# Optimization experiments

Measured on AMD Instinct MI355X. Metric: run time of the kernel, lower is better.

The kernel has to match this reference:

```python
import jax, jax.numpy as jnp
import numpy as np

B, N, D = 2, 2048, 2048
H, HKV, HD = 16, 4, 128  # n_heads, n_kv_heads, head_dim
G = H // HKV             # GQA group size


def setup_inputs() -> dict:
    key = jax.random.key(0)
    ks = jax.random.split(key, 5)
    x = jax.random.normal(ks[0], (B, N, D), jnp.float32)
    # rotary angles: standard 10000-base frequencies, half head_dim
    inv_freq = 1.0 / (10000.0 ** (jnp.arange(HD // 2, dtype=jnp.float32) / (HD // 2)))
    ang = jnp.arange(N, dtype=jnp.float32)[:, None] * inv_freq[None, :]  # [N, HD/2]
    cos = jnp.cos(ang)[None, :, None, :]  # [1, N, 1, HD/2]
    sin = jnp.sin(ang)[None, :, None, :]
    attn_mask = jnp.ones((B, N), jnp.float32)
    s = 0.02
    Wq = jax.random.normal(ks[1], (D, H * HD), jnp.float32) * s
    Wkv = jax.random.normal(ks[2], (D, 2 * HKV * HD), jnp.float32) * s
    Wo = jax.random.normal(ks[3], (H * HD, D), jnp.float32) * s
    bo = jnp.zeros((D,), jnp.float32)
    return {"x": x, "cos": cos, "sin": sin, "attn_mask": attn_mask,
            "Wq": Wq, "Wkv": Wkv, "Wo": Wo, "bo": bo}


def _rope(t, cos, sin):
    # t: [b, n, h, d]; rotate-half style split at d//2
    d2 = t.shape[-1] // 2
    t1, t2 = t[..., :d2], t[..., d2:]
    return jnp.concatenate([t1 * cos + t2 * sin, t2 * cos - t1 * sin], axis=-1)


def reference(x, cos, sin, attn_mask, Wq, Wkv, Wo, bo):
    b, n, _ = x.shape
    q = (x @ Wq).reshape(b, n, H, HD)
    kv = x @ Wkv
    k, v = jnp.split(kv, 2, axis=-1)
    k = k.reshape(b, n, HKV, HD)
    v = v.reshape(b, n, HKV, HD)
    q = _rope(q, cos, sin)
    k = _rope(k, cos, sin)
    # b n h d -> b h n d; group q heads: head H_idx maps to kv head H_idx % HKV
    # (einops '(r h)' repeat pattern => q reshaped as [b, G, HKV, n, d])
    q = q.transpose(0, 2, 1, 3).reshape(b, G, HKV, n, HD)
    k = k.transpose(0, 2, 1, 3)  # [b, HKV, n, d]
    v = v.transpose(0, 2, 1, 3)
    scale = HD ** -0.5
    attn = jnp.einsum('bghnd,bhmd->bghnm', q, k) * scale
    bias = (1.0 - attn_mask) * -1e9  # [b, n_keys]
    attn = attn + bias[:, None, None, None, :]
    attn = jax.nn.softmax(attn, axis=-1)
    out = jnp.einsum('bghnm,bhmd->bghnd', attn, v)
    # b (g h) n d -> b n (g h d)
    out = out.transpose(0, 3, 1, 2, 4).reshape(b, n, H * HD)
    return out @ Wo + bo
```

## Files before the change

### kernel.cpp

```cpp
#include <hip/hip_runtime.h>
#include <hip/hip_bf16.h>
#include <cstddef>

#define NB    2
#define NSEQ  2048
#define DMODEL 2048
#define NH    16
#define NKV   4
#define HDIM  128

typedef __attribute__((ext_vector_type(8))) short short8;
typedef __attribute__((ext_vector_type(4))) short short4v;
typedef __attribute__((ext_vector_type(4))) float floatx4;
typedef const __attribute__((address_space(1))) void* gptr_t;
typedef __attribute__((address_space(3))) void* lptr_t;

#if __has_builtin(__builtin_amdgcn_exp2f)
#define EXP2F(x) __builtin_amdgcn_exp2f(x)
#else
#define EXP2F(x) __expf((x) * 0.6931471805599453f)
#endif

__device__ inline unsigned short f2bf(float f) {
    unsigned int u = __float_as_uint(f);
    u += 0x7fffu + ((u >> 16) & 1u);
    return (unsigned short)(u >> 16);
}

__device__ inline unsigned int pk2bf_trunc(float a, float b) {
    return __builtin_amdgcn_perm(__float_as_uint(b), __float_as_uint(a), 0x07060302u);
}

__device__ inline floatx4 fzero4() {
    floatx4 v; v[0] = 0.f; v[1] = 0.f; v[2] = 0.f; v[3] = 0.f; return v;
}

__global__ void prep_k(const float* __restrict__ x, const float* __restrict__ Wq,
                       const float* __restrict__ Wkv, const float* __restrict__ Wo,
                       const float* __restrict__ mask,
                       unsigned short* __restrict__ xb,
                       unsigned short* __restrict__ W1T,
                       unsigned short* __restrict__ WoT,
                       float* __restrict__ bias2) {
    __shared__ float tile[32][33];
    const int bid = blockIdx.x, t = threadIdx.x;
    if (bid < 8192) {
        int i = bid * 256 + t;
        float4 v = ((const float4*)x)[i];
        ushort4 o;
        o.x = f2bf(v.x); o.y = f2bf(v.y); o.z = f2bf(v.z); o.w = f2bf(v.w);
        ((ushort4*)xb)[i] = o;
        return;
    }
    if (bid >= 18432) {
        int i = (bid - 18432) * 1024 + t * 4;
        float4 m = *(const float4*)(mask + i);
        const float c = -1.4426950408889634e9f;
        float4 o;
        o.x = (1.f - m.x) * c; o.y = (1.f - m.y) * c;
        o.z = (1.f - m.z) * c; o.w = (1.f - m.w) * c;
        *(float4*)(bias2 + i) = o;
        return;
    }
    const float* W; unsigned short* Wt; int N, local;
    if (bid < 12288)      { W = Wq;  Wt = W1T;                       N = 2048; local = bid - 8192; }
    else if (bid < 14336) { W = Wkv; Wt = W1T + (size_t)2048 * 2048; N = 1024; local = bid - 12288; }
    else                  { W = Wo;  Wt = WoT;                       N = 2048; local = bid - 14336; }
    const int K = 2048;
    int nt = N >> 5;
    int bx = local % nt, by = local / nt;
    int n0 = bx * 32, k0 = by * 32, tx = t & 31, ty = t >> 5;
#pragma unroll
    for (int i = 0; i < 4; i++)
        tile[ty + i * 8][tx] = W[(size_t)(k0 + ty + i * 8) * N + n0 + tx];
    __syncthreads();
#pragma unroll
    for (int i = 0; i < 4; i++)
        Wt[(size_t)(n0 + ty + i * 8) * K + k0 + tx] = f2bf(tile[tx][ty + i * 8]);
}

__global__ __launch_bounds__(256, 3) void gemm_bt(
    const unsigned short* __restrict__ A,
    const unsigned short* __restrict__ Bt,
    float* __restrict__ C,
    const float* __restrict__ bias,
    int M, int N, int K) {
    __shared__ __align__(16) unsigned short As[128 * 64];
    __shared__ __align__(16) unsigned short Bs[128 * 64];
    const int t = threadIdx.x;
    const int chunk = gridDim.x >> 3;
    const int wgid = (blockIdx.x & 7) * chunk + (blockIdx.x >> 3);
    const int nx = N >> 7;
    const int m0 = (wgid / nx) * 128, n0 = (wgid % nx) * 128;
    const int lane = t & 63, wave = t >> 6;
    const int ln = lane & 15, quad = lane >> 4;
    const int wm = (wave >> 1) * 64, wn = (wave & 1) * 64;
    floatx4 acc[4][4];
#pragma unroll
    for (int r = 0; r < 4; r++)
#pragma unroll
        for (int c = 0; c < 4; c++) acc[r][c] = fzero4();

    int xsw[2];
#pragma unroll
    for (int kc = 0; kc < 2; kc++)
        xsw[kc] = (((kc << 2) + quad) ^ (ln & 7)) * 8;

    for (int kt = 0; kt < K; kt += 64) {
#pragma unroll
        for (int i = 0; i < 4; i++) {
            int c = i * 256 + t, r = c >> 3, c8 = c & 7;
            int scol = kt + ((c8 ^ (r & 7)) * 8);
            __builtin_amdgcn_global_load_lds(
                (gptr_t)(A + (size_t)(m0 + r) * K + scol),
                (lptr_t)(As + c * 8), 16, 0, 0);
            __builtin_amdgcn_global_load_lds(
                (gptr_t)(Bt + (size_t)(n0 + r) * K + scol),
                (lptr_t)(Bs + c * 8), 16, 0, 0);
        }
        __syncthreads();
#pragma unroll
        for (int kc = 0; kc < 2; kc++) {
            short8 af[4], bfr[4];
#pragma unroll
            for (int r = 0; r < 4; r++)
                af[r] = *(const short8*)(As + (wm + r * 16 + ln) * 64 + xsw[kc]);
#pragma unroll
            for (int c = 0; c < 4; c++)
                bfr[c] = *(const short8*)(Bs + (wn + c * 16 + ln) * 64 + xsw[kc]);
#pragma unroll
            for (int r = 0; r < 4; r++)
#pragma unroll
                for (int c = 0; c < 4; c++)
                    acc[r][c] = __builtin_amdgcn_mfma_f32_16x16x32_bf16(
                        af[r], bfr[c], acc[r][c], 0, 0, 0);
        }
        __syncthreads();
    }
#pragma unroll
    for (int r = 0; r < 4; r++) {
        int mb = m0 + wm + r * 16 + quad * 4;
#pragma unroll
        for (int c = 0; c < 4; c++) {
            int col = n0 + wn + c * 16 + ln;
            float bv = bias ? bias[col] : 0.f;
#pragma unroll
            for (int g = 0; g < 4; g++)
                C[(size_t)(mb + g) * N + col] = acc[r][c][g] + bv;
        }
    }
}

__global__ __launch_bounds__(256, 3) void gemm_qkv_rope(
    const unsigned short* __restrict__ A,
    const unsigned short* __restrict__ Bt,
    const float* __restrict__ cosb,
    const float* __restrict__ sinb,
    unsigned short* __restrict__ Qb,
    unsigned short* __restrict__ Kb,
    unsigned short* __restrict__ Vt) {
    const int K = DMODEL;
    __shared__ __align__(16) unsigned char smem[128 * 136 * 2];
    unsigned short* As = (unsigned short*)smem;
    unsigned short* Bs = (unsigned short*)(smem + 16384);
    unsigned short* Vx = (unsigned short*)smem;
    const int t = threadIdx.x;
    const int wgid = (blockIdx.x & 7) * 96 + (blockIdx.x >> 3);
    const int m0 = (wgid / 24) * 128, n0 = (wgid % 24) * 128;
    const int lane = t & 63, wave = t >> 6;
    const int ln = lane & 15, quad = lane >> 4;
    const int wm = (wave >> 1) * 64, bq = (wave & 1) * 32;
    floatx4 acc[4][4];
#pragma unroll
    for (int r = 0; r < 4; r++)
#pragma unroll
        for (int c = 0; c < 4; c++) acc[r][c] = fzero4();

    int xsw[2];
#pragma unroll
    for (int kc = 0; kc < 2; kc++)
        xsw[kc] = (((kc << 2) + quad) ^ (ln & 7)) * 8;

    for (int kt = 0; kt < K; kt += 64) {
#pragma unroll
        for (int i = 0; i < 4; i++) {
            int c = i * 256 + t, r = c >> 3, c8 = c & 7;
            int scol = kt + ((c8 ^ (r & 7)) * 8);
            __builtin_amdgcn_global_load_lds(
                (gptr_t)(A + (size_t)(m0 + r) * K + scol),
                (lptr_t)(As + c * 8), 16, 0, 0);
            __builtin_amdgcn_global_load_lds(
                (gptr_t)(Bt + (size_t)(n0 + r) * K + scol),
                (lptr_t)(Bs + c * 8), 16, 0, 0);
        }
        __syncthreads();
#pragma unroll
        for (int kc = 0; kc < 2; kc++) {
            short8 af[4], bfr[4];
#pragma unroll
            for (int r = 0; r < 4; r++)
                af[r] = *(const short8*)(As + (wm + r * 16 + ln) * 64 + xsw[kc]);
#pragma unroll
            for (int c = 0; c < 4; c++)
                bfr[c] = *(const short8*)(
                    Bs + (bq + (c & 1) * 16 + (c >> 1) * 64 + ln) * 64 + xsw[kc]);
#pragma unroll
            for (int r = 0; r < 4; r++)
#pragma unroll
                for (int c = 0; c < 4; c++)
                    acc[r][c] = __builtin_amdgcn_mfma_f32_16x16x32_bf16(
                        af[r], bfr[c], acc[r][c], 0, 0, 0);
        }
        __syncthreads();
    }

    if (n0 < 2048) {
        const float qs = (float)(0.08838834764831845 * 1.4426950408889634);
        int h = n0 >> 7;
#pragma unroll
        for (int r = 0; r < 4; r++)
#pragma unroll
            for (int c = 0; c < 2; c++)
#pragma unroll
                for (int g = 0; g < 4; g++) {
                    int row = m0 + wm + r * 16 + quad * 4 + g;
                    int b = row >> 11, n = row & 2047;
                    int j = bq + c * 16 + ln;
                    float cv = cosb[n * 64 + j], sv = sinb[n * 64 + j];
                    float t1 = acc[r][c][g], t2 = acc[r][c + 2][g];
                    unsigned short* qp = Qb + ((size_t)(b * NH + h) * NSEQ + n) * 128;
                    qp[j]      = f2bf((t1 * cv + t2 * sv) * qs);
                    qp[j + 64] = f2bf((t2 * cv - t1 * sv) * qs);
                }
    } else if (n0 < 2560) {
        int hk = (n0 - 2048) >> 7;
#pragma unroll
        for (int r = 0; r < 4; r++)
#pragma unroll
            for (int c = 0; c < 2; c++)
#pragma unroll
                for (int g = 0; g < 4; g++) {
                    int row = m0 + wm + r * 16 + quad * 4 + g;
                    int b = row >> 11, n = row & 2047;
                    int j = bq + c * 16 + ln;
                    float cv = cosb[n * 64 + j], sv = sinb[n * 64 + j];
                    float t1 = acc[r][c][g], t2 = acc[r][c + 2][g];
                    unsigned short* kp = Kb + ((size_t)(b * NKV + hk) * NSEQ + n) * 128;
                    kp[j]      = f2bf(t1 * cv + t2 * sv);
                    kp[j + 64] = f2bf(t2 * cv - t1 * sv);
                }
    } else {
        int hk = (n0 - 2560) >> 7;
#pragma unroll
        for (int r = 0; r < 4; r++)
#pragma unroll
            for (int c = 0; c < 4; c++) {
                int d = bq + (c & 1) * 16 + (c >> 1) * 64 + ln;
                int s = wm + (r >> 1) * 32 + quad * 8 + (r & 1) * 4;
#pragma unroll
                for (int g = 0; g < 4; g++)
                    Vx[d * 136 + s + g] = f2bf(acc[r][c][g]);
            }
        __syncthreads();
        int b = m0 >> 11, nloc = m0 & 2047;
#pragma unroll
        for (int pass = 0; pass < 2; pass++) {
            int d = pass * 64 + (t >> 2), q4 = t & 3;
            unsigned short* vp =
                Vt + ((size_t)(b * NKV + hk) * 128 + d) * NSEQ + nloc + q4 * 32;
#pragma unroll
            for (int i = 0; i < 4; i++)
                *(short8*)(vp + i * 8) = *(const short8*)(Vx + d * 136 + q4 * 32 + i * 8);
        }
    }
}

__global__ __launch_bounds__(128, 2) void attn_k(
    const unsigned short* __restrict__ Qb,
    const unsigned short* __restrict__ Kb,
    const unsigned short* __restrict__ Vt,
    const float* __restrict__ bias2,
    unsigned short* __restrict__ Ab) {
    __shared__ __align__(16) unsigned short Ks[2 * 32 * 128];
    __shared__ __align__(16) unsigned short Vs[2 * 128 * 32];
    const int t = threadIdx.x, wave = t >> 6, lane = t & 63;
    const int ln = lane & 15, quad = lane >> 4;
    const int id = blockIdx.x;
    const int pair = id & 7, b = pair >> 2, kv = pair & 3;
    const int rest = id >> 3, g4 = rest & 3, h = g4 * 4 + kv, qb = rest >> 2;
    const int q0 = qb * 64;

    const unsigned short* Kbase = Kb + (size_t)(b * NKV + kv) * NSEQ * 128;
    const unsigned short* Vbase = Vt + (size_t)(b * NKV + kv) * 128 * NSEQ;
    const float* bbase = bias2 + b * NSEQ;

    const unsigned short* Qp =
        Qb + ((size_t)(b * NH + h) * NSEQ + q0 + wave * 32 + ln) * 128;
    short8 qf[2][4];
#pragma unroll
    for (int rt = 0; rt < 2; rt++)
#pragma unroll
        for (int kc = 0; kc < 4; kc++)
            qf[rt][kc] = *(const short8*)(Qp + rt * 16 * 128 + kc * 32 + quad * 8);

    const char* kp[4];
#pragma unroll
    for (int kc = 0; kc < 4; kc++)
        kp[kc] = (const char*)Ks + ln * 256 + (((kc * 4 + quad) ^ (ln & 7)) * 16);
    const char* vpp = (const char*)Vs + ln * 64 + ((quad ^ ((ln ^ (ln >> 2)) & 3)) * 16);

    floatx4 Oacc[2][8];
#pragma unroll
    for (int rt = 0; rt < 2; rt++)
#pragma unroll
        for (int d = 0; d < 8; d++) Oacc[rt][d] = fzero4();
    floatx4 Lacc[2];
    Lacc[0] = fzero4(); Lacc[1] = fzero4();

    short8 ones8;
#pragma unroll
    for (int i = 0; i < 8; i++) ones8[i] = (short)0x3F80;

    auto stage = [&](int ktn, int buf) {
#pragma unroll
        for (int i = 0; i < 4; i++) {
            int c = i * 128 + t, r = c >> 4, c8 = c & 15;
            __builtin_amdgcn_global_load_lds(
                (gptr_t)(Kbase + (size_t)(ktn + r) * 128 + ((c8 ^ (r & 7)) * 8)),
                (lptr_t)(Ks + buf * 4096 + c * 8), 16, 0, 0);
        }
#pragma unroll
        for (int i = 0; i < 4; i++) {
            int c = i * 128 + t, dr = c >> 2, c8 = c & 3;
            int f = (dr ^ (dr >> 2)) & 3;
            __builtin_amdgcn_global_load_lds(
                (gptr_t)(Vbase + (size_t)dr * NSEQ + ktn + ((c8 ^ f) * 8)),
                (lptr_t)(Vs + buf * 4096 + c * 8), 16, 0, 0);
        }
    };

    stage(0, 0);
    __syncthreads();

#pragma unroll 1
    for (int it2 = 0; it2 < NSEQ / 64; ++it2) {
#pragma unroll
        for (int half = 0; half < 2; ++half) {
            const int kt = (it2 * 2 + half) * 32;
            const int ktn = (kt + 32) & (NSEQ - 1);
            stage(ktn, half ^ 1);
            const int off = half * 8192;

            floatx4 sacc[2][2];
#pragma unroll
            for (int nj = 0; nj < 2; nj++) {
                floatx4 bv = *(const floatx4*)(bbase + kt + nj * 16 + quad * 4);
                sacc[0][nj] = bv;
                sacc[1][nj] = bv;
            }
            __builtin_amdgcn_s_setprio(1);
#pragma unroll
            for (int kc = 0; kc < 4; kc++) {
                short8 kfv[2];
#pragma unroll
                for (int nj = 0; nj < 2; nj++)
                    kfv[nj] = *(const short8*)(kp[kc] + off + nj * 4096);
#pragma unroll
                for (int rt = 0; rt < 2; rt++)
#pragma unroll
                    for (int nj = 0; nj < 2; nj++)
                        sacc[rt][nj] = __builtin_amdgcn_mfma_f32_16x16x32_bf16(
                            kfv[nj], qf[rt][kc], sacc[rt][nj], 0, 0, 0);
            }
            __builtin_amdgcn_s_setprio(0);

            short8 pf[2];
#pragma unroll
            for (int rt = 0; rt < 2; rt++) {
                union { short8 s; unsigned int w[4]; } pu;
#pragma unroll
                for (int e = 0; e < 2; e++) {
                    float e0 = EXP2F(sacc[rt][e][0]);
                    float e1 = EXP2F(sacc[rt][e][1]);
                    float e2 = EXP2F(sacc[rt][e][2]);
                    float e3 = EXP2F(sacc[rt][e][3]);
                    pu.w[e * 2 + 0] = pk2bf_trunc(e0, e1);
                    pu.w[e * 2 + 1] = pk2bf_trunc(e2, e3);
                }
                pf[rt] = pu.s;
            }

            __builtin_amdgcn_s_setprio(1);
#pragma unroll
            for (int rt = 0; rt < 2; rt++)
                Lacc[rt] = __builtin_amdgcn_mfma_f32_16x16x32_bf16(
                    ones8, pf[rt], Lacc[rt], 0, 0, 0);
#pragma unroll
            for (int dt = 0; dt < 8; dt++) {
                short8 vf = *(const short8*)(vpp + off + dt * 1024);
#pragma unroll
                for (int rt = 0; rt < 2; rt++)
                    Oacc[rt][dt] = __builtin_amdgcn_mfma_f32_16x16x32_bf16(
                        vf, pf[rt], Oacc[rt][dt], 0, 0, 0);
            }
            __builtin_amdgcn_s_setprio(0);
            __syncthreads();
        }
    }

#pragma unroll
    for (int rt = 0; rt < 2; rt++) {
        float inv = 1.f / Lacc[rt][0];
        int row = q0 + wave * 32 + rt * 16 + ln;
        unsigned short* outp = Ab + (size_t)(b * NSEQ + row) * 2048 + h * 128;
#pragma unroll
        for (int dt = 0; dt < 8; dt++) {
            short4v o4;
#pragma unroll
            for (int g = 0; g < 4; g++) o4[g] = (short)f2bf(Oacc[rt][dt][g] * inv);
            *(short4v*)(outp + dt * 16 + quad * 4) = o4;
        }
    }
}

extern "C" void kernel_launch(void* const* d_in, const int* in_sizes, int n_in,
                              void* d_out, int out_size, void* d_ws, size_t ws_size,
                              hipStream_t stream) {
    const float* x    = (const float*)d_in[0];
    const float* cosb = (const float*)d_in[1];
    const float* sinb = (const float*)d_in[2];
    const float* mask = (const float*)d_in[3];
    const float* Wq   = (const float*)d_in[4];
    const float* Wkv  = (const float*)d_in[5];
    const float* Wo   = (const float*)d_in[6];
    const float* bo   = (const float*)d_in[7];
    float* out = (float*)d_out;

    char* ws = (char*)d_ws;
    unsigned short* xb  = (unsigned short*)ws; ws += (size_t)4096 * 2048 * 2;
    unsigned short* W1T = (unsigned short*)ws; ws += (size_t)3072 * 2048 * 2;
    unsigned short* WoT = (unsigned short*)ws; ws += (size_t)2048 * 2048 * 2;
    unsigned short* Qb  = (unsigned short*)ws; ws += (size_t)2 * 16 * 2048 * 128 * 2;
    unsigned short* Kb  = (unsigned short*)ws; ws += (size_t)2 * 4 * 2048 * 128 * 2;
    unsigned short* Vt  = (unsigned short*)ws; ws += (size_t)2 * 4 * 2048 * 128 * 2;
    unsigned short* Ab  = (unsigned short*)ws; ws += (size_t)2 * 2048 * 2048 * 2;
    float* bias2 = (float*)ws;                 ws += (size_t)NB * NSEQ * 4;

    prep_k<<<18436, 256, 0, stream>>>(x, Wq, Wkv, Wo, mask, xb, W1T, WoT, bias2);
    gemm_qkv_rope<<<768, 256, 0, stream>>>(xb, W1T, cosb, sinb, Qb, Kb, Vt);
    attn_k<<<1024, 128, 0, stream>>>(Qb, Kb, Vt, bias2, Ab);
    gemm_bt<<<512, 256, 0, stream>>>(Ab, WoT, out, bo, 4096, 2048, 2048);
}
```

Measured before the change: 300.7 us.

## Use 512x128 tiles with triple-buffered async LDS pipeline in both GEMMs

Both projection GEMMs move to 512-thread workgroups computing 512x128 output tiles with a K-step of 32. Operands are staged through a three-slot LDS ring filled by global_load_lds, using partial vmcnt waits and raw barriers so loads overlap MFMA work, plus s_setprio around the math. This trades occupancy and grid size (192 and 128 blocks, fewer than the CU count) for more operand reuse per block and latency hiding. The V-transpose epilogue is redone in four passes to fit the larger tile.

```diff
diff --git a/kernel.cpp b/kernel.cpp
--- a/kernel.cpp
+++ b/kernel.cpp
@@ -79,79 +79,100 @@
         Wt[(size_t)(n0 + ty + i * 8) * K + k0 + tx] = f2bf(tile[tx][ty + i * 8]);
 }
 
-__global__ __launch_bounds__(256, 3) void gemm_bt(
+
+__global__ __launch_bounds__(512) void gemm_bt(
     const unsigned short* __restrict__ A,
     const unsigned short* __restrict__ Bt,
     float* __restrict__ C,
     const float* __restrict__ bias,
     int M, int N, int K) {
-    __shared__ __align__(16) unsigned short As[128 * 64];
-    __shared__ __align__(16) unsigned short Bs[128 * 64];
+    __shared__ __align__(16) unsigned short As[3 * 512 * 32];
+    __shared__ __align__(16) unsigned short Bs[3 * 128 * 32];
     const int t = threadIdx.x;
     const int chunk = gridDim.x >> 3;
     const int wgid = (blockIdx.x & 7) * chunk + (blockIdx.x >> 3);
     const int nx = N >> 7;
-    const int m0 = (wgid / nx) * 128, n0 = (wgid % nx) * 128;
+    const int m0 = (wgid / nx) * 512, n0 = (wgid % nx) * 128;
     const int lane = t & 63, wave = t >> 6;
     const int ln = lane & 15, quad = lane >> 4;
-    const int wm = (wave >> 1) * 64, wn = (wave & 1) * 64;
-    floatx4 acc[4][4];
-#pragma unroll
-    for (int r = 0; r < 4; r++)
+    const int wm = (wave >> 1) * 128, bq = (wave & 1) * 32;
+    const int xrd = (quad ^ (ln & 3) ^ ((ln >> 2) & 3)) * 8;
+    floatx4 acc[8][4];
+#pragma unroll
+    for (int r = 0; r < 8; r++)
 #pragma unroll
         for (int c = 0; c < 4; c++) acc[r][c] = fzero4();
 
-    int xsw[2];
-#pragma unroll
-    for (int kc = 0; kc < 2; kc++)
-        xsw[kc] = (((kc << 2) + quad) ^ (ln & 7)) * 8;
-
-    for (int kt = 0; kt < K; kt += 64) {
-#pragma unroll
-        for (int i = 0; i < 4; i++) {
-            int c = i * 256 + t, r = c >> 3, c8 = c & 7;
-            int scol = kt + ((c8 ^ (r & 7)) * 8);
-            __builtin_amdgcn_global_load_lds(
-                (gptr_t)(A + (size_t)(m0 + r) * K + scol),
-                (lptr_t)(As + c * 8), 16, 0, 0);
-            __builtin_amdgcn_global_load_lds(
-                (gptr_t)(Bt + (size_t)(n0 + r) * K + scol),
-                (lptr_t)(Bs + c * 8), 16, 0, 0);
-        }
-        __syncthreads();
-#pragma unroll
-        for (int kc = 0; kc < 2; kc++) {
-            short8 af[4], bfr[4];
-#pragma unroll
-            for (int r = 0; r < 4; r++)
-                af[r] = *(const short8*)(As + (wm + r * 16 + ln) * 64 + xsw[kc]);
-#pragma unroll
-            for (int c = 0; c < 4; c++)
-                bfr[c] = *(const short8*)(Bs + (wn + c * 16 + ln) * 64 + xsw[kc]);
-#pragma unroll
-            for (int r = 0; r < 4; r++)
-#pragma unroll
-                for (int c = 0; c < 4; c++)
-                    acc[r][c] = __builtin_amdgcn_mfma_f32_16x16x32_bf16(
-                        af[r], bfr[c], acc[r][c], 0, 0, 0);
-        }
-        __syncthreads();
-    }
-#pragma unroll
-    for (int r = 0; r < 4; r++) {
+    auto stage = [&](int kt, int buf) {
+#pragma unroll
+        for (int j = 0; j < 4; ++j) {
+            int c = j * 512 + t, r = c >> 2, c4 = c & 3;
+            int sx = (c4 ^ (r & 3) ^ ((r >> 2) & 3)) * 8;
+            __builtin_amdgcn_global_load_lds(
+                (gptr_t)(A + (size_t)(m0 + r) * K + kt + sx),
+                (lptr_t)(As + buf * 16384 + c * 8), 16, 0, 0);
+        }
+        {
+            int c = t, r = c >> 2, c4 = c & 3;
+            int sx = (c4 ^ (r & 3) ^ ((r >> 2) & 3)) * 8;
+            __builtin_amdgcn_global_load_lds(
+                (gptr_t)(Bt + (size_t)(n0 + r) * K + kt + sx),
+                (lptr_t)(Bs + buf * 4096 + c * 8), 16, 0, 0);
+        }
+    };
+
+    stage(0, 0);
+    stage(32, 1);
+    asm volatile("s_waitcnt vmcnt(5)" ::: "memory");
+    __builtin_amdgcn_s_barrier();
+
+    int cur = 0, tgt = 2;
+#pragma unroll 1
+    for (int i = 0; i < K / 32; ++i) {
+        const int ktn = ((i + 2) * 32) & (K - 1);
+        stage(ktn, tgt);
+        const unsigned short* Ab_ = As + cur * 16384;
+        const unsigned short* Bb_ = Bs + cur * 4096;
+        short8 bfr[4];
+#pragma unroll
+        for (int c = 0; c < 4; ++c)
+            bfr[c] = *(const short8*)(Ab_ - Ab_ + Bb_ + (bq + (c & 1) * 16 + (c >> 1) * 64 + ln) * 32 + xrd);
+        __builtin_amdgcn_s_setprio(1);
+#pragma unroll
+        for (int ha = 0; ha < 2; ++ha) {
+            short8 af[4];
+#pragma unroll
+            for (int rr = 0; rr < 4; ++rr)
+                af[rr] = *(const short8*)(Ab_ + (wm + (ha * 4 + rr) * 16 + ln) * 32 + xrd);
+#pragma unroll
+            for (int rr = 0; rr < 4; ++rr)
+#pragma unroll
+                for (int c = 0; c < 4; ++c)
+                    acc[ha * 4 + rr][c] = __builtin_amdgcn_mfma_f32_16x16x32_bf16(
+                        af[rr], bfr[c], acc[ha * 4 + rr][c], 0, 0, 0);
+        }
+        __builtin_amdgcn_s_setprio(0);
+        asm volatile("s_waitcnt vmcnt(5)" ::: "memory");
+        __builtin_amdgcn_s_barrier();
+        cur = (cur == 2) ? 0 : cur + 1;
+        tgt = (tgt == 2) ? 0 : tgt + 1;
+    }
+
+#pragma unroll
+    for (int r = 0; r < 8; ++r) {
         int mb = m0 + wm + r * 16 + quad * 4;
 #pragma unroll
-        for (int c = 0; c < 4; c++) {
-            int col = n0 + wn + c * 16 + ln;
+        for (int c = 0; c < 4; ++c) {
+            int col = n0 + bq + (c & 1) * 16 + (c >> 1) * 64 + ln;
             float bv = bias ? bias[col] : 0.f;
 #pragma unroll
-            for (int g = 0; g < 4; g++)
+            for (int g = 0; g < 4; ++g)
                 C[(size_t)(mb + g) * N + col] = acc[r][c][g] + bv;
         }
     }
 }
 
-__global__ __launch_bounds__(256, 3) void gemm_qkv_rope(
+__global__ __launch_bounds__(512) void gemm_qkv_rope(
     const unsigned short* __restrict__ A,
     const unsigned short* __restrict__ Bt,
     const float* __restrict__ cosb,
@@ -160,65 +181,83 @@
     unsigned short* __restrict__ Kb,
     unsigned short* __restrict__ Vt) {
     const int K = DMODEL;
-    __shared__ __align__(16) unsigned char smem[128 * 136 * 2];
+    __shared__ __align__(16) unsigned char smem[122880];
     unsigned short* As = (unsigned short*)smem;
-    unsigned short* Bs = (unsigned short*)(smem + 16384);
+    unsigned short* Bs = (unsigned short*)(smem + 98304);
     unsigned short* Vx = (unsigned short*)smem;
     const int t = threadIdx.x;
-    const int wgid = (blockIdx.x & 7) * 96 + (blockIdx.x >> 3);
-    const int m0 = (wgid / 24) * 128, n0 = (wgid % 24) * 128;
+    const int wgid = (blockIdx.x & 7) * 24 + (blockIdx.x >> 3);
+    const int m0 = (wgid / 24) * 512, n0 = (wgid % 24) * 128;
     const int lane = t & 63, wave = t >> 6;
     const int ln = lane & 15, quad = lane >> 4;
-    const int wm = (wave >> 1) * 64, bq = (wave & 1) * 32;
-    floatx4 acc[4][4];
-#pragma unroll
-    for (int r = 0; r < 4; r++)
+    const int wm = (wave >> 1) * 128, bq = (wave & 1) * 32;
+    const int xrd = (quad ^ (ln & 3) ^ ((ln >> 2) & 3)) * 8;
+    floatx4 acc[8][4];
+#pragma unroll
+    for (int r = 0; r < 8; r++)
 #pragma unroll
         for (int c = 0; c < 4; c++) acc[r][c] = fzero4();
 
-    int xsw[2];
-#pragma unroll
-    for (int kc = 0; kc < 2; kc++)
-        xsw[kc] = (((kc << 2) + quad) ^ (ln & 7)) * 8;
-
-    for (int kt = 0; kt < K; kt += 64) {
-#pragma unroll
-        for (int i = 0; i < 4; i++) {
-            int c = i * 256 + t, r = c >> 3, c8 = c & 7;
-            int scol = kt + ((c8 ^ (r & 7)) * 8);
-            __builtin_amdgcn_global_load_lds(
-                (gptr_t)(A + (size_t)(m0 + r) * K + scol),
-                (lptr_t)(As + c * 8), 16, 0, 0);
-            __builtin_amdgcn_global_load_lds(
-                (gptr_t)(Bt + (size_t)(n0 + r) * K + scol),
-                (lptr_t)(Bs + c * 8), 16, 0, 0);
-        }
-        __syncthreads();
-#pragma unroll
-        for (int kc = 0; kc < 2; kc++) {
-            short8 af[4], bfr[4];
-#pragma unroll
-            for (int r = 0; r < 4; r++)
-                af[r] = *(const short8*)(As + (wm + r * 16 + ln) * 64 + xsw[kc]);
-#pragma unroll
-            for (int c = 0; c < 4; c++)
-                bfr[c] = *(const short8*)(
-                    Bs + (bq + (c & 1) * 16 + (c >> 1) * 64 + ln) * 64 + xsw[kc]);
-#pragma unroll
-            for (int r = 0; r < 4; r++)
-#pragma unroll
-                for (int c = 0; c < 4; c++)
-                    acc[r][c] = __builtin_amdgcn_mfma_f32_16x16x32_bf16(
-                        af[r], bfr[c], acc[r][c], 0, 0, 0);
-        }
-        __syncthreads();
+    auto stage = [&](int kt, int buf) {
+#pragma unroll
+        for (int j = 0; j < 4; ++j) {
+            int c = j * 512 + t, r = c >> 2, c4 = c & 3;
+            int sx = (c4 ^ (r & 3) ^ ((r >> 2) & 3)) * 8;
+            __builtin_amdgcn_global_load_lds(
+                (gptr_t)(A + (size_t)(m0 + r) * K + kt + sx),
+                (lptr_t)(As + buf * 16384 + c * 8), 16, 0, 0);
+        }
+        {
+            int c = t, r = c >> 2, c4 = c & 3;
+            int sx = (c4 ^ (r & 3) ^ ((r >> 2) & 3)) * 8;
+            __builtin_amdgcn_global_load_lds(
+                (gptr_t)(Bt + (size_t)(n0 + r) * K + kt + sx),
+                (lptr_t)(Bs + buf * 4096 + c * 8), 16, 0, 0);
+        }
+    };
+
+    stage(0, 0);
+    stage(32, 1);
+    asm volatile("s_waitcnt vmcnt(5)" ::: "memory");
+    __builtin_amdgcn_s_barrier();
+
+    int cur = 0, tgt = 2;
+#pragma unroll 1
+    for (int i = 0; i < K / 32; ++i) {
+        const int ktn = ((i + 2) * 32) & (K - 1);
+        stage(ktn, tgt);
+        const unsigned short* Ab_ = As + cur * 16384;
+        const unsigned short* Bb_ = Bs + cur * 4096;
+        short8 bfr[4];
+#pragma unroll
+        for (int c = 0; c < 4; ++c)
+            bfr[c] = *(const short8*)(Bb_ + (bq + (c & 1) * 16 + (c >> 1) * 64 + ln) * 32 + xrd);
+        __builtin_amdgcn_s_setprio(1);
+#pragma unroll
+        for (int ha = 0; ha < 2; ++ha) {
+            short8 af[4];
+#pragma unroll
+            for (int rr = 0; rr < 4; ++rr)
+                af[rr] = *(const short8*)(Ab_ + (wm + (ha * 4 + rr) * 16 + ln) * 32 + xrd);
+#pragma unroll
+            for (int rr = 0; rr < 4; ++rr)
+#pragma unroll
+                for (int c = 0; c < 4; ++c)
+                    acc[ha * 4 + rr][c] = __builtin_amdgcn_mfma_f32_16x16x32_bf16(
+                        af[rr], bfr[c], acc[ha * 4 + rr][c], 0, 0, 0);
+        }
+        __builtin_amdgcn_s_setprio(0);
+        asm volatile("s_waitcnt vmcnt(5)" ::: "memory");
+        __builtin_amdgcn_s_barrier();
+        cur = (cur == 2) ? 0 : cur + 1;
+        tgt = (tgt == 2) ? 0 : tgt + 1;
     }
 
     if (n0 < 2048) {
         const float qs = (float)(0.08838834764831845 * 1.4426950408889634);
         int h = n0 >> 7;
 #pragma unroll
-        for (int r = 0; r < 4; r++)
+        for (int r = 0; r < 8; r++)
 #pragma unroll
             for (int c = 0; c < 2; c++)
 #pragma unroll
@@ -235,7 +274,7 @@
     } else if (n0 < 2560) {
         int hk = (n0 - 2048) >> 7;
 #pragma unroll
-        for (int r = 0; r < 4; r++)
+        for (int r = 0; r < 8; r++)
 #pragma unroll
             for (int c = 0; c < 2; c++)
 #pragma unroll
@@ -251,26 +290,32 @@
                 }
     } else {
         int hk = (n0 - 2560) >> 7;
-#pragma unroll
-        for (int r = 0; r < 4; r++)
-#pragma unroll
-            for (int c = 0; c < 4; c++) {
-                int d = bq + (c & 1) * 16 + (c >> 1) * 64 + ln;
-                int s = wm + (r >> 1) * 32 + quad * 8 + (r & 1) * 4;
-#pragma unroll
-                for (int g = 0; g < 4; g++)
-                    Vx[d * 136 + s + g] = f2bf(acc[r][c][g]);
+        asm volatile("s_waitcnt vmcnt(0)" ::: "memory");
+        __syncthreads();
+        int b = m0 >> 11;
+#pragma unroll 1
+        for (int p = 0; p < 4; ++p) {
+            if ((wave >> 1) == p) {
+#pragma unroll
+                for (int r = 0; r < 8; r++)
+#pragma unroll
+                    for (int c = 0; c < 4; c++) {
+                        int d = bq + (c & 1) * 16 + (c >> 1) * 64 + ln;
+                        int s = (r >> 2) * 64 + ((r & 3) >> 1) * 32 + quad * 8 + (r & 1) * 4;
+#pragma unroll
+                        for (int g = 0; g < 4; g++)
+                            Vx[d * 136 + s + g] = f2bf(acc[r][c][g]);
+                    }
             }
-        __syncthreads();
-        int b = m0 >> 11, nloc = m0 & 2047;
-#pragma unroll
-        for (int pass = 0; pass < 2; pass++) {
-            int d = pass * 64 + (t >> 2), q4 = t & 3;
+            __syncthreads();
+            int nloc = (m0 & 2047) + p * 128;
+            int d = t >> 2, q4 = t & 3;
             unsigned short* vp =
                 Vt + ((size_t)(b * NKV + hk) * 128 + d) * NSEQ + nloc + q4 * 32;
 #pragma unroll
-            for (int i = 0; i < 4; i++)
-                *(short8*)(vp + i * 8) = *(const short8*)(Vx + d * 136 + q4 * 32 + i * 8);
+            for (int i2 = 0; i2 < 4; i2++)
+                *(short8*)(vp + i2 * 8) = *(const short8*)(Vx + d * 136 + q4 * 32 + i2 * 8);
+            __syncthreads();
         }
     }
 }
@@ -447,7 +492,7 @@
     float* bias2 = (float*)ws;                 ws += (size_t)NB * NSEQ * 4;
 
     prep_k<<<18436, 256, 0, stream>>>(x, Wq, Wkv, Wo, mask, xb, W1T, WoT, bias2);
-    gemm_qkv_rope<<<768, 256, 0, stream>>>(xb, W1T, cosb, sinb, Qb, Kb, Vt);
+    gemm_qkv_rope<<<192, 512, 0, stream>>>(xb, W1T, cosb, sinb, Qb, Kb, Vt);
     attn_k<<<1024, 128, 0, stream>>>(Qb, Kb, Vt, bias2, Ab);
-    gemm_bt<<<512, 256, 0, stream>>>(Ab, WoT, out, bo, 4096, 2048, 2048);
-}
+    gemm_bt<<<128, 512, 0, stream>>>(Ab, WoT, out, bo, 4096, 2048, 2048);
+}
```

Measured after the change: 355.4 us. 1.18x slower.
